# Kernel tuning notes

Hardware: AMD Instinct MI355X
Metric: run time of the kernel (lower is better)

## Reference

```python
import jax, jax.numpy as jnp
import numpy as np

SP = 4          # split_size
HEADS = 8       # num_heads
SHIFTS = (0, 2) # shift_sizes


def _to_windows(t, nh, hs, nw, ws, heads):
    # 'b (c head) (nh hs) (nw ws) -> (b nh nw) head (hs ws) c'
    B, C, H, W = t.shape
    hd = C // heads
    t = t.reshape(B, hd, heads, nh, hs, nw, ws)
    t = t.transpose(0, 3, 5, 2, 4, 6, 1)  # B, nh, nw, heads, hs, ws, hd
    return t.reshape(B * nh * nw, heads, hs * ws, hd)


def _from_windows(t, B, nh, hs, nw, ws, heads):
    # '(b nh nw) head (hs ws) c -> b (c head) (nh hs) (nw ws)'
    hd = t.shape[-1]
    t = t.reshape(B, nh, nw, heads, hs, ws, hd)
    t = t.transpose(0, 6, 3, 1, 4, 2, 5)  # B, hd, heads, nh, hs, nw, ws
    return t.reshape(B, hd * heads, nh * hs, nw * ws)


def _dwconv3(v, w, b):
    # depthwise 3x3, padding 1 (groups = channels)
    out = jax.lax.conv_general_dilated(
        v, w, window_strides=(1, 1), padding=((1, 1), (1, 1)),
        dimension_numbers=('NCHW', 'OIHW', 'NCHW'),
        feature_group_count=v.shape[1])
    return out + b[None, :, None, None]


def setup_inputs() -> dict:
    key = jax.random.key(0)
    k1, k2, k3, k4 = jax.random.split(key, 4)
    B, C, H, W = 8, 256, 64, 64
    sd = C // 2
    x = jax.random.normal(k1, (B, C, H, W), dtype=jnp.float32)
    w_qkv = jax.random.normal(k2, (3 * sd, sd, 1, 1), dtype=jnp.float32) * 0.05
    w_lepe = jax.random.normal(k3, (sd, 1, 3, 3), dtype=jnp.float32) * 0.1
    b_lepe = jax.random.normal(k4, (sd,), dtype=jnp.float32) * 0.01
    return {"x": x, "w_qkv": w_qkv, "w_lepe": w_lepe, "b_lepe": b_lepe}


def reference(x, w_qkv, w_lepe, b_lepe):
    B, C, H, W = x.shape
    sd = C // 2
    scale = (sd // HEADS) ** -0.5
    wq = w_qkv[:, :, 0, 0]  # [3*sd, sd]
    outs = []
    for s in SHIFTS:
        # NOTE: original rolls dims (1,2) = (channels, height)
        xs = jnp.roll(x, (-s, -s), axis=(1, 2)) if s > 0 else x
        parts = []
        # vertical strips (full-H, width SP), horizontal strips (height SP, full-W)
        strip_params = [(1, H, W // SP, SP), (H // SP, SP, 1, W)]
        for idx, (nh, hs, nw, ws) in enumerate(strip_params):
            xsp = xs[:, idx * sd:(idx + 1) * sd]  # channel half
            qkv = jnp.einsum('bchw,oc->bohw', xsp, wq)
            q, k, v = qkv[:, :sd], qkv[:, sd:2 * sd], qkv[:, 2 * sd:]
            lepe = _dwconv3(v, w_lepe, b_lepe)
            qw = _to_windows(q, nh, hs, nw, ws, HEADS) * scale
            kw = _to_windows(k, nh, hs, nw, ws, HEADS)
            vw = _to_windows(v, nh, hs, nw, ws, HEADS)
            lw = _to_windows(lepe, nh, hs, nw, ws, HEADS)
            attn = jax.nn.softmax(jnp.einsum('whqc,whkc->whqk', qw, kw), axis=-1)
            ow = jnp.einsum('whqk,whkc->whqc', attn, vw) + lw
            o = _from_windows(ow, B, nh, hs, nw, ws, HEADS)
            if s > 0:
                o = jnp.roll(o, (s, s), axis=(1, 2))
            parts.append(o)
        outs.append(jnp.concatenate(parts, axis=1))
    return outs[0] + outs[1]
```

## Files before the change

kernel.cpp:

```cpp
#include <hip/hip_runtime.h>
#include <hip/hip_bf16.h>

typedef _Float16 f16;
typedef _Float16 half4 __attribute__((ext_vector_type(4)));
typedef float floatx4 __attribute__((ext_vector_type(4)));

#define WIN 4194304


__global__ void k_prep(const float* __restrict__ wq, f16* __restrict__ wqB) {
    int D = blockIdx.x * 256 + threadIdx.x;
    if (D >= 49152) return;
    int kj = D & 3, lane = (D >> 2) & 63, nt = (D >> 8) & 7;
    int kt = (D >> 11) & 7, part = D >> 14;
    int g = lane >> 4, ln = lane & 15;
    int o = part * 128 + nt * 16 + ln;
    int k = kt * 16 + g * 4 + kj;
    wqB[D] = (f16)wq[o * 128 + k];
}

__global__ __launch_bounds__(256, 2) void k_proj(
    const float* __restrict__ x, const f16* __restrict__ wqB,
    f16* __restrict__ qw, f16* __restrict__ kw, f16* __restrict__ vw, int s)
{
    const int rt = blockIdx.x, b = blockIdx.y, idx = blockIdx.z;
    const int h0 = rt * 2;
    const int tid = threadIdx.x;
    const int wave = tid >> 6, lane = tid & 63, g = lane >> 4, ln = lane & 15;

    union __align__(16) SM {
        f16 xa[32 * 128 * 4];
        f16 pt[128 * 136];
    };
    __shared__ SM sm;

    for (int ii = tid; ii < 4096; ii += 256) {
        int c = ii >> 5, j = ii & 31;
        int row = j >> 4, w4 = (j & 15) << 2;
        int gc = (idx * 128 + c + s) & 255;
        int gh = (h0 + row + s) & 63;
        float4 v4 = *(const float4*)&x[(((size_t)b * 256 + gc) << 12) + (gh << 6) + w4];
        const float* vp = (const float*)&v4;
        int m0 = (row << 6) + w4;
        #pragma unroll
        for (int jj = 0; jj < 4; ++jj)
            sm.xa[((c >> 2) * 128 + m0 + jj) * 4 + (c & 3)] = (f16)vp[jj];
    }
    __syncthreads();

    half4 af[2][8];
    #pragma unroll
    for (int mt = 0; mt < 2; ++mt)
        #pragma unroll
        for (int kt = 0; kt < 8; ++kt) {
            int m = wave * 32 + mt * 16 + ln;
            af[mt][kt] = *(const half4*)&sm.xa[((kt * 4 + g) * 128 + m) * 4];
        }

    for (int part = 0; part < 3; ++part) {
        floatx4 C[8][2];
        #pragma unroll
        for (int nt = 0; nt < 8; ++nt)
            #pragma unroll
            for (int mt = 0; mt < 2; ++mt) C[nt][mt] = (floatx4){0.f, 0.f, 0.f, 0.f};

        for (int kt = 0; kt < 8; ++kt) {
            half4 bf[8];
            #pragma unroll
            for (int nt = 0; nt < 8; ++nt)
                bf[nt] = *(const half4*)&wqB[((((part * 8 + kt) * 8 + nt) * 64) + lane) * 4];
            #pragma unroll
            for (int nt = 0; nt < 8; ++nt)
                #pragma unroll
                for (int mt = 0; mt < 2; ++mt)
                    C[nt][mt] = __builtin_amdgcn_mfma_f32_16x16x16f16(
                        af[mt][kt], bf[nt], C[nt][mt], 0, 0, 0);
        }

        const float qsc = (part == 0) ? 0.25f * 1.4426950408889634f : 1.0f;

        __syncthreads();
        #pragma unroll
        for (int nt = 0; nt < 8; ++nt)
            #pragma unroll
            for (int mt = 0; mt < 2; ++mt)
                #pragma unroll
                for (int r = 0; r < 4; ++r) {
                    int m = wave * 32 + mt * 16 + g * 4 + r;
                    int c = nt * 16 + ln;
                    int hc = ((c & 7) << 4) + (c >> 3);
                    f16 hv = (f16)(C[nt][mt][r] * qsc);
                    if (part == 2) sm.pt[hc * 136 + m] = hv;
                    else           sm.pt[m * 136 + hc] = hv;
                }
        __syncthreads();

        if (part < 2) {
            f16* dst = (part == 0 ? qw : kw) + (size_t)idx * WIN;
            int tq = tid >> 4, hcg = tid & 15;
            #pragma unroll
            for (int it = 0; it < 8; ++it) {
                int m = it * 16 + tq;
                int h = h0 + (m >> 6), w = m & 63;
                int winG, t;
                if (idx == 0) { winG = b * 16 + (w >> 2); t = (h << 2) | (w & 3); }
                else          { winG = b * 16 + (h >> 2); t = ((h & 3) << 6) | w; }
                *(float4*)(dst + (((size_t)winG * 256 + t) << 7) + hcg * 8) =
                    *(const float4*)&sm.pt[m * 136 + hcg * 8];
            }
        } else {
            f16* dst = vw + (size_t)idx * WIN;
            int mg = tid & 15, hcq = tid >> 4;
            int row = mg >> 3, h = h0 + row;
            #pragma unroll
            for (int it = 0; it < 8; ++it) {
                int hc = it * 16 + hcq;
                if (idx == 1) {
                    int w = (mg & 7) * 8;
                    int winG = b * 16 + (h >> 2);
                    int t = ((h & 3) << 6) | w;
                    *(float4*)(dst + (((size_t)winG * 128 + hc) << 8) + t) =
                        *(const float4*)&sm.pt[hc * 136 + mg * 8];
                } else {
                    #pragma unroll
                    for (int q2 = 0; q2 < 2; ++q2) {
                        int w0 = (mg & 7) * 8 + q2 * 4;
                        int winG = b * 16 + (w0 >> 2);
                        int t = h << 2;
                        *(half4*)(dst + (((size_t)winG * 128 + hc) << 8) + t) =
                            *(const half4*)&sm.pt[hc * 136 + mg * 8 + q2 * 4];
                    }
                }
            }
        }
    }
}

__global__ __launch_bounds__(256) void k_lepe(
    const f16* __restrict__ vw, const float* __restrict__ wle,
    const float* __restrict__ ble, f16* __restrict__ lepe)
{
    const int winG = blockIdx.x, idx = blockIdx.y, hg = blockIdx.z;
    const int wi = winG & 15;
    const int tid = threadIdx.x;
    const int hc0 = hg * 8;
    const f16* vb = vw + (size_t)idx * WIN;
    f16* lb = lepe + (size_t)idx * WIN;

    __shared__ f16 sp[4096];

    if (idx == 0) {
        for (int ii = tid; ii < 8 * 256; ii += 256) {
            int hcl = ii >> 8, t = ii & 255;
            f16 v = vb[(((size_t)winG * 128 + hc0 + hcl) << 8) + t];
            sp[(hcl << 9) + ((t >> 2) << 3) + 1 + (t & 3)] = v;
        }
        for (int ii = tid; ii < 8 * 128; ii += 256) {
            int hcl = ii >> 7, j = ii & 127;
            int side = j >> 6, h = j & 63;
            f16 v = (f16)0.f;
            if (side == 0) { if (wi > 0)
                v = vb[(((size_t)(winG - 1) * 128 + hc0 + hcl) << 8) + h * 4 + 3]; }
            else           { if (wi < 15)
                v = vb[(((size_t)(winG + 1) * 128 + hc0 + hcl) << 8) + h * 4]; }
            sp[(hcl << 9) + (h << 3) + (side ? 5 : 0)] = v;
        }
        __syncthreads();
        int h = tid >> 2, wp = 1 + (tid & 3);
        for (int hcl = 0; hcl < 8; ++hcl) {
            int hc = hc0 + hcl, d = hc & 15, head = hc >> 4;
            int c = d * 8 + head;
            float acc = ble[c];
            #pragma unroll
            for (int ky = 0; ky < 3; ++ky) {
                int hh = h + ky - 1;
                if (hh < 0 || hh > 63) continue;
                #pragma unroll
                for (int kx = 0; kx < 3; ++kx)
                    acc = fmaf(wle[c * 9 + ky * 3 + kx],
                               (float)sp[(hcl << 9) + (hh << 3) + wp + kx - 1], acc);
            }
            lb[(((size_t)winG * 128 + hc) << 8) + tid] = (f16)acc;
        }
    } else {
        const int ROW = 68;
        for (int ii = tid; ii < 8 * 256; ii += 256) {
            int hcl = ii >> 8, t = ii & 255;
            f16 v = vb[(((size_t)winG * 128 + hc0 + hcl) << 8) + t];
            sp[hcl * 6 * ROW + (1 + (t >> 6)) * ROW + 1 + (t & 63)] = v;
        }
        for (int ii = tid; ii < 8 * 128; ii += 256) {
            int hcl = ii >> 7, j = ii & 127;
            int side = j >> 6, w = j & 63;
            f16 v = (f16)0.f;
            if (side == 0) { if (wi > 0)
                v = vb[(((size_t)(winG - 1) * 128 + hc0 + hcl) << 8) + 192 + w]; }
            else           { if (wi < 15)
                v = vb[(((size_t)(winG + 1) * 128 + hc0 + hcl) << 8) + w]; }
            sp[hcl * 6 * ROW + (side ? 5 : 0) * ROW + 1 + w] = v;
        }
        for (int ii = tid; ii < 8 * 6 * 2; ii += 256) {
            int hcl = ii / 12, rr = (ii % 12) >> 1, e = ii & 1;
            sp[hcl * 6 * ROW + rr * ROW + (e ? 65 : 0)] = (f16)0.f;
        }
        __syncthreads();
        int hloc = tid >> 6, w = tid & 63;
        for (int hcl = 0; hcl < 8; ++hcl) {
            int hc = hc0 + hcl, d = hc & 15, head = hc >> 4;
            int c = d * 8 + head;
            float acc = ble[c];
            #pragma unroll
            for (int ky = 0; ky < 3; ++ky)
                #pragma unroll
                for (int kx = 0; kx < 3; ++kx)
                    acc = fmaf(wle[c * 9 + ky * 3 + kx],
                               (float)sp[hcl * 6 * ROW + (hloc + ky) * ROW + w + kx],
                               acc);
            lb[(((size_t)winG * 128 + hc) << 8) + tid] = (f16)acc;
        }
    }
}

__global__ __launch_bounds__(256) void k_attn(
    const f16* __restrict__ qw, const f16* __restrict__ kw,
    const f16* __restrict__ vw, const f16* __restrict__ lep,
    f16* __restrict__ ow)
{
    const int tid = threadIdx.x;
    const int lane = tid & 63, wave = tid >> 6;
    const int g = lane >> 4, ln = lane & 15;
    const int head = blockIdx.x & 7, idx = (blockIdx.x >> 3) & 1;
    const int winG = blockIdx.x >> 4;

    __shared__ f16 kl[4096];
    __shared__ f16 vl[4096];

    const size_t cb = ((size_t)(winG * 8 + head)) << 4;
    const f16* qb = qw + (size_t)idx * WIN + ((size_t)winG << 15) + head * 16;
    const f16* kb = kw + (size_t)idx * WIN + ((size_t)winG << 15) + head * 16;
    const f16* vb = vw + (size_t)idx * WIN;
    const f16* lb = lep + (size_t)idx * WIN;
    f16* ob = ow + (size_t)idx * WIN;

    {
        int t = tid;
        const f16* src = kb + ((size_t)t << 7);
        float4 a = *(const float4*)src;
        float4 b2 = *(const float4*)(src + 8);
        const f16* ap = (const f16*)&a;
        const f16* bp = (const f16*)&b2;
        int kt = t >> 4, l2 = t & 15;
        *(half4*)&kl[(kt * 64 + 0 * 16 + l2) * 4] = *(const half4*)(ap);
        *(half4*)&kl[(kt * 64 + 1 * 16 + l2) * 4] = *(const half4*)(ap + 4);
        *(half4*)&kl[(kt * 64 + 2 * 16 + l2) * 4] = *(const half4*)(bp);
        *(half4*)&kl[(kt * 64 + 3 * 16 + l2) * 4] = *(const half4*)(bp + 4);
    }
    {
        const f16* src = vb + (cb << 8);
        #pragma unroll
        for (int r2 = 0; r2 < 2; ++r2) {
            int e = r2 * 256 + tid;
            float4 a = *(const float4*)(src + e * 8);
            const f16* ap = (const f16*)&a;
            int d = e >> 5;
            int t0 = (e & 31) * 8;
            int kt0 = t0 >> 4, g0 = (t0 >> 2) & 3;
            *(half4*)&vl[(kt0 * 64 + g0 * 16 + d) * 4] = *(const half4*)ap;
            int t1 = t0 + 4;
            int kt1 = t1 >> 4, g1 = (t1 >> 2) & 3;
            *(half4*)&vl[(kt1 * 64 + g1 * 16 + d) * 4] = *(const half4*)(ap + 4);
        }
    }

    half4 qf[4];
    #pragma unroll
    for (int qt = 0; qt < 4; ++qt) {
        int t = wave * 64 + qt * 16 + ln;
        qf[qt] = *(const half4*)(qb + ((size_t)t << 7) + g * 4);
    }

    __syncthreads();

    floatx4 o[4]; float lsum[4];
    #pragma unroll
    for (int qt = 0; qt < 4; ++qt) { o[qt] = (floatx4){0.f,0.f,0.f,0.f}; lsum[qt] = 0.f; }

    for (int kt = 0; kt < 16; ++kt) {
        half4 kf = *(const half4*)&kl[(kt * 64 + lane) * 4];
        half4 vf = *(const half4*)&vl[(kt * 64 + lane) * 4];
        #pragma unroll
        for (int qt = 0; qt < 4; ++qt) {
            floatx4 sc = __builtin_amdgcn_mfma_f32_16x16x16f16(
                kf, qf[qt], (floatx4){0.f,0.f,0.f,0.f}, 0, 0, 0);
            float p0 = __builtin_amdgcn_exp2f(sc[0]);
            float p1 = __builtin_amdgcn_exp2f(sc[1]);
            float p2 = __builtin_amdgcn_exp2f(sc[2]);
            float p3 = __builtin_amdgcn_exp2f(sc[3]);
            lsum[qt] += (p0 + p1) + (p2 + p3);
            half4 pf = {(f16)p0, (f16)p1, (f16)p2, (f16)p3};
            o[qt] = __builtin_amdgcn_mfma_f32_16x16x16f16(vf, pf, o[qt], 0, 0, 0);
        }
    }

    #pragma unroll
    for (int qt = 0; qt < 4; ++qt) {
        float l = lsum[qt];
        l += __shfl_xor(l, 16);
        l += __shfl_xor(l, 32);
        float inv = 1.f / l;
        int t = wave * 64 + qt * 16 + ln;
        #pragma unroll
        for (int r = 0; r < 4; ++r) {
            int d = g * 4 + r;
            float val = fmaf(o[qt][r], inv, (float)lb[((cb + d) << 8) + t]);
            ob[((cb + d) << 8) + t] = (f16)val;
        }
    }
}

__global__ __launch_bounds__(256) void k_final(
    const f16* __restrict__ ow0, const f16* __restrict__ ow2,
    float* __restrict__ out)
{
    #pragma unroll
    for (int it = 0; it < 4; ++it) {
        int e = blockIdx.x * 1024 + it * 256 + threadIdx.x;
        int w = e & 63, oh = (e >> 6) & 63, oc = (e >> 12) & 255, b = e >> 20;
        float acc = 0.f;
        #pragma unroll
        for (int si = 0; si < 2; ++si) {
            int s = si * 2;
            const f16* p = si ? ow2 : ow0;
            int idx = oc >> 7;
            int cl = ((oc & 127) - s) & 127;
            int h = (oh - s) & 63;
            int head = cl & 7, d = cl >> 3;
            int wg, t;
            if (idx == 0) { wg = b * 16 + (w >> 2); t = (h << 2) | (w & 3); }
            else          { wg = b * 16 + (h >> 2); t = ((h & 3) << 6) | w; }
            acc += (float)p[(size_t)idx * WIN
                            + (((size_t)(wg * 8 + head) * 16 + d) << 8) + t];
        }
        out[e] = acc;
    }
}

extern "C" void kernel_launch(void* const* d_in, const int* in_sizes, int n_in,
                              void* d_out, int out_size, void* d_ws, size_t ws_size,
                              hipStream_t stream) {
    const float* x      = (const float*)d_in[0];
    const float* w_qkv  = (const float*)d_in[1];
    const float* w_lepe = (const float*)d_in[2];
    const float* b_lepe = (const float*)d_in[3];
    float* out = (float*)d_out;

    f16* wsf = (f16*)d_ws;
    f16* wqB = wsf;
    f16* qw  = wsf + 65536;
    f16* kw  = qw + 2 * (size_t)WIN;
    f16* vw  = kw + 2 * (size_t)WIN;
    f16* lep = vw + 2 * (size_t)WIN;
    f16* ow0 = lep + 2 * (size_t)WIN;
    f16* ow2 = lep;

    k_prep<<<192, 256, 0, stream>>>(w_qkv, wqB);

    k_proj<<<dim3(32, 8, 2), 256, 0, stream>>>(x, wqB, qw, kw, vw, 0);
    k_lepe<<<dim3(128, 2, 16), 256, 0, stream>>>(vw, w_lepe, b_lepe, lep);
    k_attn<<<2048, 256, 0, stream>>>(qw, kw, vw, lep, ow0);

    k_proj<<<dim3(32, 8, 2), 256, 0, stream>>>(x, wqB, qw, kw, vw, 2);
    k_lepe<<<dim3(128, 2, 16), 256, 0, stream>>>(vw, w_lepe, b_lepe, lep);
    k_attn<<<2048, 256, 0, stream>>>(qw, kw, vw, lep, ow2);

    k_final<<<8192, 256, 0, stream>>>(ow0, ow2, out);
}
```

Measured before the change: 259.7 us.

## Batch both shift passes into single launches and swizzle projection LDS staging

```diff
diff --git a/kernel.cpp b/kernel.cpp
--- a/kernel.cpp
+++ b/kernel.cpp
@@ -6,7 +6,7 @@
 typedef float floatx4 __attribute__((ext_vector_type(4)));
 
 #define WIN 4194304
-
+#define SSTR 41943040
 
 __global__ void k_prep(const float* __restrict__ wq, f16* __restrict__ wqB) {
     int D = blockIdx.x * 256 + threadIdx.x;
@@ -21,9 +21,12 @@
 
 __global__ __launch_bounds__(256, 2) void k_proj(
     const float* __restrict__ x, const f16* __restrict__ wqB,
-    f16* __restrict__ qw, f16* __restrict__ kw, f16* __restrict__ vw, int s)
+    f16* __restrict__ qw, f16* __restrict__ kw, f16* __restrict__ vw)
 {
-    const int rt = blockIdx.x, b = blockIdx.y, idx = blockIdx.z;
+    const int rt = blockIdx.x, b = blockIdx.y;
+    const int idx = blockIdx.z & 1, si = blockIdx.z >> 1;
+    const int s = si * 2;
+    const size_t so = (size_t)si * SSTR;
     const int h0 = rt * 2;
     const int tid = threadIdx.x;
     const int wave = tid >> 6, lane = tid & 63, g = lane >> 4, ln = lane & 15;
@@ -34,28 +37,50 @@
     };
     __shared__ SM sm;
 
-    for (int ii = tid; ii < 4096; ii += 256) {
-        int c = ii >> 5, j = ii & 31;
-        int row = j >> 4, w4 = (j & 15) << 2;
-        int gc = (idx * 128 + c + s) & 255;
-        int gh = (h0 + row + s) & 63;
-        float4 v4 = *(const float4*)&x[(((size_t)b * 256 + gc) << 12) + (gh << 6) + w4];
-        const float* vp = (const float*)&v4;
-        int m0 = (row << 6) + w4;
-        #pragma unroll
-        for (int jj = 0; jj < 4; ++jj)
-            sm.xa[((c >> 2) * 128 + m0 + jj) * 4 + (c & 3)] = (f16)vp[jj];
+    {
+        const int wg = tid & 31;
+        const int row = wg >> 4, w4 = (wg & 15) << 2;
+        const int gh = (h0 + row + s) & 63;
+        const int m0 = row * 64 + w4;
+        const unsigned fb = (((unsigned)m0 >> 4) & 7u) << 4;
+        const float* xp = x + (((size_t)b * 256) << 12) + (gh << 6) + w4;
+        char* lbase = (char*)sm.xa;
+        #pragma unroll
+        for (int it = 0; it < 4; ++it) {
+            int cg = (tid >> 5) + it * 8;
+            float4 v4[4];
+            #pragma unroll
+            for (int cc = 0; cc < 4; ++cc) {
+                int gc = (idx * 128 + cg * 4 + cc + s) & 255;
+                v4[cc] = *(const float4*)(xp + ((size_t)gc << 12));
+            }
+            union { half4 h[4]; float4 q[2]; } t;
+            #pragma unroll
+            for (int jj = 0; jj < 4; ++jj)
+                t.h[jj] = (half4){
+                    (f16)(((const float*)&v4[0])[jj]),
+                    (f16)(((const float*)&v4[1])[jj]),
+                    (f16)(((const float*)&v4[2])[jj]),
+                    (f16)(((const float*)&v4[3])[jj])};
+            char* p = lbase + cg * 1024;
+            *(float4*)(p + (((unsigned)(m0 * 8)) ^ fb)) = t.q[0];
+            *(float4*)(p + (((unsigned)(m0 * 8 + 16)) ^ fb)) = t.q[1];
+        }
     }
     __syncthreads();
 
     half4 af[2][8];
     #pragma unroll
-    for (int mt = 0; mt < 2; ++mt)
+    for (int mt = 0; mt < 2; ++mt) {
+        int m = wave * 32 + mt * 16 + ln;
+        unsigned fb = (((unsigned)m >> 4) & 7u) << 4;
         #pragma unroll
         for (int kt = 0; kt < 8; ++kt) {
-            int m = wave * 32 + mt * 16 + ln;
-            af[mt][kt] = *(const half4*)&sm.xa[((kt * 4 + g) * 128 + m) * 4];
-        }
+            int kc = kt * 4 + g;
+            af[mt][kt] = *(const half4*)((char*)sm.xa + kc * 1024 +
+                                         (((unsigned)(m * 8)) ^ fb));
+        }
+    }
 
     for (int part = 0; part < 3; ++part) {
         floatx4 C[8][2];
@@ -96,7 +121,7 @@
         __syncthreads();
 
         if (part < 2) {
-            f16* dst = (part == 0 ? qw : kw) + (size_t)idx * WIN;
+            f16* dst = (part == 0 ? qw : kw) + so + (size_t)idx * WIN;
             int tq = tid >> 4, hcg = tid & 15;
             #pragma unroll
             for (int it = 0; it < 8; ++it) {
@@ -109,7 +134,7 @@
                     *(const float4*)&sm.pt[m * 136 + hcg * 8];
             }
         } else {
-            f16* dst = vw + (size_t)idx * WIN;
+            f16* dst = vw + so + (size_t)idx * WIN;
             int mg = tid & 15, hcq = tid >> 4;
             int row = mg >> 3, h = h0 + row;
             #pragma unroll
@@ -140,12 +165,14 @@
     const f16* __restrict__ vw, const float* __restrict__ wle,
     const float* __restrict__ ble, f16* __restrict__ lepe)
 {
-    const int winG = blockIdx.x, idx = blockIdx.y, hg = blockIdx.z;
+    const int winG = blockIdx.x, hg = blockIdx.z;
+    const int idx = blockIdx.y & 1, si = blockIdx.y >> 1;
+    const size_t so = (size_t)si * SSTR;
     const int wi = winG & 15;
     const int tid = threadIdx.x;
     const int hc0 = hg * 8;
-    const f16* vb = vw + (size_t)idx * WIN;
-    f16* lb = lepe + (size_t)idx * WIN;
+    const f16* vb = vw + so + (size_t)idx * WIN;
+    f16* lb = lepe + so + (size_t)idx * WIN;
 
     __shared__ f16 sp[4096];
 
@@ -230,17 +257,19 @@
     const int lane = tid & 63, wave = tid >> 6;
     const int g = lane >> 4, ln = lane & 15;
     const int head = blockIdx.x & 7, idx = (blockIdx.x >> 3) & 1;
-    const int winG = blockIdx.x >> 4;
+    const int winG = (blockIdx.x >> 4) & 127;
+    const int si = blockIdx.x >> 11;
+    const size_t so = (size_t)si * SSTR;
 
     __shared__ f16 kl[4096];
     __shared__ f16 vl[4096];
 
     const size_t cb = ((size_t)(winG * 8 + head)) << 4;
-    const f16* qb = qw + (size_t)idx * WIN + ((size_t)winG << 15) + head * 16;
-    const f16* kb = kw + (size_t)idx * WIN + ((size_t)winG << 15) + head * 16;
-    const f16* vb = vw + (size_t)idx * WIN;
-    const f16* lb = lep + (size_t)idx * WIN;
-    f16* ob = ow + (size_t)idx * WIN;
+    const f16* qb = qw + so + (size_t)idx * WIN + ((size_t)winG << 15) + head * 16;
+    const f16* kb = kw + so + (size_t)idx * WIN + ((size_t)winG << 15) + head * 16;
+    const f16* vb = vw + so + (size_t)idx * WIN;
+    const f16* lb = lep + so + (size_t)idx * WIN;
+    f16* ob = ow + so + (size_t)idx * WIN;
 
     {
         int t = tid;
@@ -355,23 +384,19 @@
     float* out = (float*)d_out;
 
     f16* wsf = (f16*)d_ws;
-    f16* wqB = wsf;
-    f16* qw  = wsf + 65536;
-    f16* kw  = qw + 2 * (size_t)WIN;
-    f16* vw  = kw + 2 * (size_t)WIN;
-    f16* lep = vw + 2 * (size_t)WIN;
-    f16* ow0 = lep + 2 * (size_t)WIN;
-    f16* ow2 = lep;
+    f16* wqB  = wsf;
+    f16* base = wsf + 65536;
+    f16* qw   = base;
+    f16* kw   = base + 2 * (size_t)WIN;
+    f16* vw   = base + 4 * (size_t)WIN;
+    f16* lep  = base + 6 * (size_t)WIN;
+    f16* ow   = base + 8 * (size_t)WIN;
 
     k_prep<<<192, 256, 0, stream>>>(w_qkv, wqB);
 
-    k_proj<<<dim3(32, 8, 2), 256, 0, stream>>>(x, wqB, qw, kw, vw, 0);
-    k_lepe<<<dim3(128, 2, 16), 256, 0, stream>>>(vw, w_lepe, b_lepe, lep);
-    k_attn<<<2048, 256, 0, stream>>>(qw, kw, vw, lep, ow0);
-
-    k_proj<<<dim3(32, 8, 2), 256, 0, stream>>>(x, wqB, qw, kw, vw, 2);
-    k_lepe<<<dim3(128, 2, 16), 256, 0, stream>>>(vw, w_lepe, b_lepe, lep);
-    k_attn<<<2048, 256, 0, stream>>>(qw, kw, vw, lep, ow2);
-
-    k_final<<<8192, 256, 0, stream>>>(ow0, ow2, out);
-}
+    k_proj<<<dim3(32, 8, 4), 256, 0, stream>>>(x, wqB, qw, kw, vw);
+    k_lepe<<<dim3(128, 4, 16), 256, 0, stream>>>(vw, w_lepe, b_lepe, lep);
+    k_attn<<<4096, 256, 0, stream>>>(qw, kw, vw, lep, ow);
+
+    k_final<<<8192, 256, 0, stream>>>(ow, ow + (size_t)SSTR, out);
+}
```

Result: faster. 233.1 us (-10.3%).
